# Optimization experiments

Measured on AMD Instinct MI355X. Metric: run time of the kernel, lower is better.

The kernel has to match this reference:

```python
import jax, jax.numpy as jnp
import numpy as np

NUM_HEADS = 4


def setup_inputs() -> dict:
    key = jax.random.key(0)
    ks = jax.random.split(key, 8)
    B, N, C = 4096, 49, 128  # num_windows*batch, Wh*Ww, embed_dims
    nW = 64                  # windows per image
    x = jax.random.normal(ks[0], (B, N, C), dtype=jnp.float32)
    mask = jax.random.normal(ks[1], (nW, N, N), dtype=jnp.float32)
    w_qkv = jax.random.normal(ks[2], (3 * C, C), dtype=jnp.float32) * (C ** -0.5)
    b_qkv = jax.random.normal(ks[3], (3 * C,), dtype=jnp.float32) * 0.02
    w_proj = jax.random.normal(ks[4], (C, C), dtype=jnp.float32) * (C ** -0.5)
    b_proj = jax.random.normal(ks[5], (C,), dtype=jnp.float32) * 0.02
    bias_table = jax.random.normal(ks[6], (169, NUM_HEADS), dtype=jnp.float32) * 0.02
    rel_index = jax.random.randint(ks[7], (N, N), 0, 169, dtype=jnp.int64)
    return {"x": x, "mask": mask, "w_qkv": w_qkv, "b_qkv": b_qkv,
            "w_proj": w_proj, "b_proj": b_proj,
            "bias_table": bias_table, "rel_index": rel_index}


def reference(x, mask, w_qkv, b_qkv, w_proj, b_proj, bias_table, rel_index):
    B, N, C = x.shape
    H = NUM_HEADS
    D = C // H
    scale = D ** -0.5
    # qkv projection: (B,N,3C) -> (3,B,H,N,D)
    qkv = (x @ w_qkv.T + b_qkv).reshape(B, N, 3, H, D).transpose(2, 0, 3, 1, 4)
    q, k, v = qkv[0], qkv[1], qkv[2]
    attn = jnp.einsum('bhnd,bhmd->bhnm', q * scale, k)  # (B,H,N,N)
    # gathered relative-position bias: (N,N,H) -> (H,N,N)
    rpb = bias_table[rel_index.reshape(-1)].reshape(N, N, H).transpose(2, 0, 1)
    attn = attn + rpb[None]
    # shift-window mask: (nW,N,N) broadcast over batch-per-window and heads
    nW = mask.shape[0]
    attn = attn.reshape(B // nW, nW, H, N, N) + mask[None, :, None]
    attn = attn.reshape(B, H, N, N)
    attn = jax.nn.softmax(attn, axis=-1)  # attn_drop is identity in eval
    out = jnp.einsum('bhnm,bhmd->bhnd', attn, v)
    out = out.transpose(0, 2, 1, 3).reshape(B, N, C)
    out = out @ w_proj.T + b_proj  # proj_drop is identity in eval
    return out
```

## Files before the change

kernel.cpp:

```cpp
#include <hip/hip_runtime.h>
#include <hip/hip_bf16.h>

typedef __attribute__((ext_vector_type(4))) float f32x4;
typedef __attribute__((ext_vector_type(8))) __bf16 bf16x8;
typedef __attribute__((ext_vector_type(4))) __bf16 bf16x4;

#define MFMA_BF16(a, b, c) __builtin_amdgcn_mfma_f32_16x16x32_bf16((a), (b), (c), 0, 0, 0)

static __device__ __forceinline__ __bf16 f2b(float f) {
    return __builtin_bit_cast(__bf16, __float2bfloat16(f));
}
static __device__ __forceinline__ unsigned short f2u(float f) {
    return __builtin_bit_cast(unsigned short, __float2bfloat16(f));
}

__global__ void prep_kernel(const float* __restrict__ w_qkv, const float* __restrict__ b_qkv,
                            const float* __restrict__ w_proj, const float* __restrict__ mask,
                            const float* __restrict__ table, const int* __restrict__ rel,
                            unsigned short* __restrict__ wqkv_b, unsigned short* __restrict__ wproj_b,
                            float* __restrict__ bqkv_s, float* __restrict__ cmb) {
    const float s = 0.17677669529663687f;
    int i = blockIdx.x * 256 + threadIdx.x;
    if (i < 49152) {
        int n = i >> 7;
        wqkv_b[i] = f2u(w_qkv[i] * (n < 128 ? s : 1.0f));
    } else if (i < 49536) {
        int j = i - 49152;
        bqkv_s[j] = b_qkv[j] * (j < 128 ? s : 1.0f);
    } else if (i < 65920) {
        int e = i - 49536;
        wproj_b[e] = f2u(w_proj[e]);
    } else if (i < 680576) {
        int c = i - 65920;
        int wi = c / 9604;
        int r2 = c - wi * 9604;
        int h = r2 / 2401;
        int mn = r2 - h * 2401;
        cmb[c] = mask[wi * 2401 + mn] + table[rel[mn] * 4 + h];
    }
}

static __device__ __forceinline__ int qk_addr(int t, int off) {
    return (t * 64 + off) ^ ((t & 7) << 4);
}

__global__ __launch_bounds__(512, 4) void fused_kernel(
    const float* __restrict__ x, const unsigned short* __restrict__ wqkv_b,
    const float* __restrict__ bqkv_s, const unsigned short* __restrict__ wproj_b,
    const float* __restrict__ b_proj, const float* __restrict__ cmb,
    float* __restrict__ out) {
    __shared__ __align__(16) char smem[65536];

    const int b = blockIdx.x;
    const int tid = threadIdx.x;
    const int lane = tid & 63;
    const int w = tid >> 6;
    const int h = w >> 1;
    const int q = w & 1;
    const int wi = b & 63;

    char* xos = smem;
    char* qkp = smem + 16384 + h * 12288;
    char* vts = qkp + 8192;

    const int rb = (lane >> 4) * 4;
    const int cI = lane & 15;

    {
        const float* xb = x + (size_t)b * 49 * 128;
        for (int i = tid; i < 2048; i += 512) {
            int row = i >> 5, c4 = (i & 31) * 4;
            float4 v = {0.f, 0.f, 0.f, 0.f};
            if (row < 49) v = *(const float4*)(xb + row * 128 + c4);
            bf16x4 bv = {f2b(v.x), f2b(v.y), f2b(v.z), f2b(v.w)};
            *(bf16x4*)(xos + row * 256 + ((c4 * 2) ^ ((row & 7) << 4))) = bv;
        }
    }
    __syncthreads();

    {
        bf16x8 af[4][4];
#pragma unroll
        for (int mt = 0; mt < 4; ++mt)
#pragma unroll
            for (int kc = 0; kc < 4; ++kc) {
                int row = mt * 16 + cI;
                af[mt][kc] = *(const bf16x8*)(xos + row * 256 +
                                              ((kc * 64 + (lane >> 4) * 16) ^ ((row & 7) << 4)));
            }
#pragma unroll
        for (int t3 = 0; t3 < 3; ++t3) {
            int n0 = t3 * 128 + w * 16;
            bf16x8 bfr[4];
#pragma unroll
            for (int kc = 0; kc < 4; ++kc)
                bfr[kc] = *(const bf16x8*)(wqkv_b + (size_t)(n0 + cI) * 128 + kc * 32 +
                                           (lane >> 4) * 8);
            f32x4 acc[4] = {};
#pragma unroll
            for (int mt = 0; mt < 4; ++mt)
#pragma unroll
                for (int kc = 0; kc < 4; ++kc)
                    acc[mt] = MFMA_BF16(af[mt][kc], bfr[kc], acc[mt]);
            float bias = bqkv_s[n0 + cI];
            int dl = q * 16 + cI;
            if (t3 < 2) {
                char* base = qkp + t3 * 4096;
#pragma unroll
                for (int mt = 0; mt < 4; ++mt)
#pragma unroll
                    for (int r = 0; r < 4; ++r) {
                        int t = mt * 16 + rb + r;
                        *(__bf16*)(base + qk_addr(t, dl * 2)) = f2b(acc[mt][r] + bias);
                    }
            } else {
#pragma unroll
                for (int mt = 0; mt < 4; ++mt) {
                    int t0 = mt * 16 + rb;
                    bf16x4 pv = {f2b(acc[mt][0] + bias), f2b(acc[mt][1] + bias),
                                 f2b(acc[mt][2] + bias), f2b(acc[mt][3] + bias)};
                    *(bf16x4*)(vts + dl * 128 + ((t0 * 2) ^ ((dl & 7) << 4))) = pv;
                }
            }
        }
    }
    __syncthreads();

    f32x4 S[2][4] = {};
    {
        bf16x8 qf[2], kf[4];
#pragma unroll
        for (int j = 0; j < 2; ++j) {
            int row = (2 * q + j) * 16 + cI;
            qf[j] = *(const bf16x8*)(qkp + qk_addr(row, (lane >> 4) * 16));
        }
#pragma unroll
        for (int nt = 0; nt < 4; ++nt) {
            int row = nt * 16 + cI;
            kf[nt] = *(const bf16x8*)(qkp + 4096 + qk_addr(row, (lane >> 4) * 16));
        }
#pragma unroll
        for (int j = 0; j < 2; ++j)
#pragma unroll
            for (int nt = 0; nt < 4; ++nt)
                S[j][nt] = MFMA_BF16(qf[j], kf[nt], S[j][nt]);
    }
    __syncthreads();
    {
        const float* cw = cmb + ((size_t)wi * 4 + h) * 2401;
#pragma unroll
        for (int j = 0; j < 2; ++j)
#pragma unroll
            for (int nt = 0; nt < 4; ++nt)
#pragma unroll
                for (int r = 0; r < 4; ++r) {
                    int m = (2 * q + j) * 16 + rb + r, n = nt * 16 + cI;
                    if (m < 49 && n < 49)
                        S[j][nt][r] += cw[m * 49 + n];
                    else
                        S[j][nt][r] = -1e30f;
                }
    }
    float sm[2][4];
#pragma unroll
    for (int j = 0; j < 2; ++j)
#pragma unroll
        for (int r = 0; r < 4; ++r) {
            float v = fmaxf(fmaxf(S[j][0][r], S[j][1][r]), fmaxf(S[j][2][r], S[j][3][r]));
            v = fmaxf(v, __shfl_xor(v, 1));
            v = fmaxf(v, __shfl_xor(v, 2));
            v = fmaxf(v, __shfl_xor(v, 4));
            v = fmaxf(v, __shfl_xor(v, 8));
            sm[j][r] = v;
        }
#pragma unroll
    for (int j = 0; j < 2; ++j)
#pragma unroll
        for (int nt = 0; nt < 4; ++nt)
#pragma unroll
            for (int r = 0; r < 4; ++r)
                S[j][nt][r] = __expf(S[j][nt][r] - sm[j][r]);
#pragma unroll
    for (int j = 0; j < 2; ++j)
#pragma unroll
        for (int r = 0; r < 4; ++r) {
            float v = S[j][0][r] + S[j][1][r] + S[j][2][r] + S[j][3][r];
            v += __shfl_xor(v, 1);
            v += __shfl_xor(v, 2);
            v += __shfl_xor(v, 4);
            v += __shfl_xor(v, 8);
            sm[j][r] = 1.0f / v;
        }
#pragma unroll
    for (int j = 0; j < 2; ++j)
#pragma unroll
        for (int nt = 0; nt < 4; ++nt)
#pragma unroll
            for (int r = 0; r < 4; ++r) {
                int m = (2 * q + j) * 16 + rb + r, n = nt * 16 + cI;
                *(__bf16*)(qkp + m * 128 + ((n * 2) ^ ((m & 7) << 4))) = f2b(S[j][nt][r]);
            }

    f32x4 Oa[2][2] = {};
#pragma unroll
    for (int kt = 0; kt < 2; ++kt) {
        const int kb = kt * 64 + (lane >> 4) * 16;
        bf16x8 pf[2], vf[2];
#pragma unroll
        for (int j = 0; j < 2; ++j) {
            int row = (2 * q + j) * 16 + cI;
            pf[j] = *(const bf16x8*)(qkp + row * 128 + (kb ^ ((row & 7) << 4)));
        }
#pragma unroll
        for (int nd = 0; nd < 2; ++nd) {
            int row = nd * 16 + cI;
            vf[nd] = *(const bf16x8*)(vts + row * 128 + (kb ^ ((row & 7) << 4)));
        }
#pragma unroll
        for (int j = 0; j < 2; ++j)
#pragma unroll
            for (int nd = 0; nd < 2; ++nd)
                Oa[j][nd] = MFMA_BF16(pf[j], vf[nd], Oa[j][nd]);
    }

#pragma unroll
    for (int j = 0; j < 2; ++j)
#pragma unroll
        for (int nd = 0; nd < 2; ++nd)
#pragma unroll
            for (int r = 0; r < 4; ++r) {
                int t = (2 * q + j) * 16 + rb + r;
                int c = h * 32 + nd * 16 + cI;
                *(__bf16*)(xos + t * 256 + ((c * 2) ^ ((t & 7) << 4))) =
                    f2b(Oa[j][nd][r] * sm[j][r]);
            }
    __syncthreads();

    {
        bf16x8 af[4][4];
#pragma unroll
        for (int mt = 0; mt < 4; ++mt)
#pragma unroll
            for (int kc = 0; kc < 4; ++kc) {
                int row = mt * 16 + cI;
                af[mt][kc] = *(const bf16x8*)(xos + row * 256 +
                                              ((kc * 64 + (lane >> 4) * 16) ^ ((row & 7) << 4)));
            }
        int n0 = w * 16;
        bf16x8 bfr[4];
#pragma unroll
        for (int kc = 0; kc < 4; ++kc)
            bfr[kc] = *(const bf16x8*)(wproj_b + (size_t)(n0 + cI) * 128 + kc * 32 +
                                       (lane >> 4) * 8);
        f32x4 acc[4] = {};
#pragma unroll
        for (int mt = 0; mt < 4; ++mt)
#pragma unroll
            for (int kc = 0; kc < 4; ++kc)
                acc[mt] = MFMA_BF16(af[mt][kc], bfr[kc], acc[mt]);
        float bias = b_proj[n0 + cI];
#pragma unroll
        for (int mt = 0; mt < 4; ++mt)
#pragma unroll
            for (int r = 0; r < 4; ++r) {
                int t = mt * 16 + rb + r;
                if (t < 49)
                    out[((size_t)b * 49 + t) * 128 + n0 + cI] = acc[mt][r] + bias;
            }
    }
}

extern "C" void kernel_launch(void* const* d_in, const int* in_sizes, int n_in,
                              void* d_out, int out_size, void* d_ws, size_t ws_size,
                              hipStream_t stream) {
    (void)in_sizes; (void)n_in; (void)out_size; (void)ws_size;
    const float* x      = (const float*)d_in[0];
    const float* mask   = (const float*)d_in[1];
    const float* w_qkv  = (const float*)d_in[2];
    const float* b_qkv  = (const float*)d_in[3];
    const float* w_proj = (const float*)d_in[4];
    const float* b_proj = (const float*)d_in[5];
    const float* btab   = (const float*)d_in[6];
    const int*   rel    = (const int*)d_in[7];
    float* out = (float*)d_out;

    char* ws = (char*)d_ws;
    unsigned short* wqkv_b  = (unsigned short*)(ws);
    unsigned short* wproj_b = (unsigned short*)(ws + 98304);
    float*          bqkv_s  = (float*)(ws + 131072);
    float*          cmb     = (float*)(ws + 132608);

    prep_kernel<<<2659, 256, 0, stream>>>(w_qkv, b_qkv, w_proj, mask, btab, rel,
                                          wqkv_b, wproj_b, bqkv_s, cmb);
    fused_kernel<<<4096, 512, 0, stream>>>(x, wqkv_b, bqkv_s, wproj_b, b_proj, cmb, out);
}
```

Measured before the change: 294.5 us.

## Use exp2 softmax without max pass, prefetch mask bias, prioritize MFMA waves

Folds log2(e) into the query scale and the precombined mask+relative-bias table so softmax can use the hardware exp2 directly. The row-max reduction and subtraction are dropped, and the reciprocal uses rcp. The mask/bias values are loaded into registers before the QK barrier to hide global latency, and s_setprio brackets the MFMA loops. Skipping the max subtraction risks overflow if scores or masks grow large.

```diff
diff --git a/kernel.cpp b/kernel.cpp
--- a/kernel.cpp
+++ b/kernel.cpp
@@ -19,7 +19,8 @@
                             const float* __restrict__ table, const int* __restrict__ rel,
                             unsigned short* __restrict__ wqkv_b, unsigned short* __restrict__ wproj_b,
                             float* __restrict__ bqkv_s, float* __restrict__ cmb) {
-    const float s = 0.17677669529663687f;
+    const float s = 0.25503485577994937f;
+    const float l2e = 1.4426950408889634f;
     int i = blockIdx.x * 256 + threadIdx.x;
     if (i < 49152) {
         int n = i >> 7;
@@ -36,7 +37,7 @@
         int r2 = c - wi * 9604;
         int h = r2 / 2401;
         int mn = r2 - h * 2401;
-        cmb[c] = mask[wi * 2401 + mn] + table[rel[mn] * 4 + h];
+        cmb[c] = (mask[wi * 2401 + mn] + table[rel[mn] * 4 + h]) * l2e;
     }
 }
 
@@ -97,11 +98,13 @@
                 bfr[kc] = *(const bf16x8*)(wqkv_b + (size_t)(n0 + cI) * 128 + kc * 32 +
                                            (lane >> 4) * 8);
             f32x4 acc[4] = {};
+            __builtin_amdgcn_s_setprio(1);
 #pragma unroll
             for (int mt = 0; mt < 4; ++mt)
 #pragma unroll
                 for (int kc = 0; kc < 4; ++kc)
                     acc[mt] = MFMA_BF16(af[mt][kc], bfr[kc], acc[mt]);
+            __builtin_amdgcn_s_setprio(0);
             float bias = bqkv_s[n0 + cI];
             int dl = q * 16 + cI;
             if (t3 < 2) {
@@ -124,6 +127,20 @@
             }
         }
     }
+
+    float cmbv[2][4][4];
+    {
+        const float* cw = cmb + ((size_t)wi * 4 + h) * 2401;
+#pragma unroll
+        for (int j = 0; j < 2; ++j)
+#pragma unroll
+            for (int nt = 0; nt < 4; ++nt)
+#pragma unroll
+                for (int r = 0; r < 4; ++r) {
+                    int m = (2 * q + j) * 16 + rb + r, n = nt * 16 + cI;
+                    cmbv[j][nt][r] = cw[(m < 49 && n < 49) ? m * 49 + n : 0];
+                }
+    }
     __syncthreads();
 
     f32x4 S[2][4] = {};
@@ -139,47 +156,27 @@
             int row = nt * 16 + cI;
             kf[nt] = *(const bf16x8*)(qkp + 4096 + qk_addr(row, (lane >> 4) * 16));
         }
+        __builtin_amdgcn_s_setprio(1);
 #pragma unroll
         for (int j = 0; j < 2; ++j)
 #pragma unroll
             for (int nt = 0; nt < 4; ++nt)
                 S[j][nt] = MFMA_BF16(qf[j], kf[nt], S[j][nt]);
-    }
-    __syncthreads();
-    {
-        const float* cw = cmb + ((size_t)wi * 4 + h) * 2401;
-#pragma unroll
-        for (int j = 0; j < 2; ++j)
-#pragma unroll
-            for (int nt = 0; nt < 4; ++nt)
-#pragma unroll
-                for (int r = 0; r < 4; ++r) {
-                    int m = (2 * q + j) * 16 + rb + r, n = nt * 16 + cI;
-                    if (m < 49 && n < 49)
-                        S[j][nt][r] += cw[m * 49 + n];
-                    else
-                        S[j][nt][r] = -1e30f;
-                }
-    }
+        __builtin_amdgcn_s_setprio(0);
+    }
+    __syncthreads();
+
+#pragma unroll
+    for (int j = 0; j < 2; ++j)
+#pragma unroll
+        for (int nt = 0; nt < 4; ++nt)
+#pragma unroll
+            for (int r = 0; r < 4; ++r) {
+                int m = (2 * q + j) * 16 + rb + r, n = nt * 16 + cI;
+                float sv = (m < 49 && n < 49) ? S[j][nt][r] + cmbv[j][nt][r] : -1e30f;
+                S[j][nt][r] = __builtin_amdgcn_exp2f(sv);
+            }
     float sm[2][4];
-#pragma unroll
-    for (int j = 0; j < 2; ++j)
-#pragma unroll
-        for (int r = 0; r < 4; ++r) {
-            float v = fmaxf(fmaxf(S[j][0][r], S[j][1][r]), fmaxf(S[j][2][r], S[j][3][r]));
-            v = fmaxf(v, __shfl_xor(v, 1));
-            v = fmaxf(v, __shfl_xor(v, 2));
-            v = fmaxf(v, __shfl_xor(v, 4));
-            v = fmaxf(v, __shfl_xor(v, 8));
-            sm[j][r] = v;
-        }
-#pragma unroll
-    for (int j = 0; j < 2; ++j)
-#pragma unroll
-        for (int nt = 0; nt < 4; ++nt)
-#pragma unroll
-            for (int r = 0; r < 4; ++r)
-                S[j][nt][r] = __expf(S[j][nt][r] - sm[j][r]);
 #pragma unroll
     for (int j = 0; j < 2; ++j)
 #pragma unroll
@@ -189,7 +186,8 @@
             v += __shfl_xor(v, 2);
             v += __shfl_xor(v, 4);
             v += __shfl_xor(v, 8);
-            sm[j][r] = 1.0f / v;
+            float inv = __builtin_amdgcn_rcpf(v);
+            sm[j][r] = (v > 0.f) ? inv : 0.f;
         }
 #pragma unroll
     for (int j = 0; j < 2; ++j)
@@ -216,11 +214,13 @@
             int row = nd * 16 + cI;
             vf[nd] = *(const bf16x8*)(vts + row * 128 + (kb ^ ((row & 7) << 4)));
         }
+        __builtin_amdgcn_s_setprio(1);
 #pragma unroll
         for (int j = 0; j < 2; ++j)
 #pragma unroll
             for (int nd = 0; nd < 2; ++nd)
                 Oa[j][nd] = MFMA_BF16(pf[j], vf[nd], Oa[j][nd]);
+        __builtin_amdgcn_s_setprio(0);
     }
 
 #pragma unroll
@@ -253,11 +253,13 @@
             bfr[kc] = *(const bf16x8*)(wproj_b + (size_t)(n0 + cI) * 128 + kc * 32 +
                                        (lane >> 4) * 8);
         f32x4 acc[4] = {};
+        __builtin_amdgcn_s_setprio(1);
 #pragma unroll
         for (int mt = 0; mt < 4; ++mt)
 #pragma unroll
             for (int kc = 0; kc < 4; ++kc)
                 acc[mt] = MFMA_BF16(af[mt][kc], bfr[kc], acc[mt]);
+        __builtin_amdgcn_s_setprio(0);
         float bias = b_proj[n0 + cI];
 #pragma unroll
         for (int mt = 0; mt < 4; ++mt)
```

Measured after the change: 416.6 us. +41.5%, slower.
